# Kernel tuning notes

Hardware: AMD Instinct MI355X
Metric: run time of the kernel (lower is better)

Reference implementation:

```python
import math
import jax, jax.numpy as jnp
import numpy as np

B, S, D, H = 2, 2048, 1024, 16
HD = D // H  # 64


def setup_inputs() -> dict:
    key = jax.random.key(0)
    k = jax.random.split(key, 8)
    x = jax.random.normal(k[0], (B, S, D), dtype=jnp.float32)
    # RoPE tables: inv_freq over half dim, emb = concat(freqs, freqs)
    inv_freq = 1.0 / (10000.0 ** (jnp.arange(0, HD, 2, dtype=jnp.float32) / HD))
    pos = jnp.arange(S, dtype=jnp.float32)
    freqs = pos[:, None] * inv_freq[None, :]            # [S, HD/2]
    emb = jnp.concatenate([freqs, freqs], axis=-1)      # [S, HD]
    cos = jnp.cos(emb)[:, None, :]                      # [S, 1, HD] broadcasts over [B,S,H,HD]
    sin = jnp.sin(emb)[:, None, :]
    # causal additive mask [1, 1, S, S]
    neg = jnp.finfo(jnp.float32).min
    mask = jnp.where(jnp.tril(jnp.ones((S, S), dtype=bool)), 0.0, neg)[None, None]
    scale = 0.02
    wq = jax.random.normal(k[1], (D, D), dtype=jnp.float32) * scale
    wk = jax.random.normal(k[2], (D, D), dtype=jnp.float32) * scale
    wv = jax.random.normal(k[3], (D, D), dtype=jnp.float32) * scale
    wo = jax.random.normal(k[4], (D, D), dtype=jnp.float32) * scale
    return {"x": x, "cos": cos, "sin": sin, "mask": mask,
            "wq": wq, "wk": wk, "wv": wv, "wo": wo}


def rotate_half(t):
    t1, t2 = t[..., : t.shape[-1] // 2], t[..., t.shape[-1] // 2:]
    return jnp.concatenate([-t2, t1], axis=-1)


def reference(x, cos, sin, mask, wq, wk, wv, wo):
    b, s, d = x.shape
    # torch nn.Linear: y = x @ W^T  (W is [out, in])
    q = (x @ wq.T).reshape(b, s, H, HD)
    kk = (x @ wk.T).reshape(b, s, H, HD)
    v = (x @ wv.T).reshape(b, s, H, HD)
    q = q * cos + rotate_half(q) * sin
    kk = kk * cos + rotate_half(kk) * sin
    q = q.transpose(0, 2, 1, 3)   # [b, h, s, hd]
    kk = kk.transpose(0, 2, 1, 3)
    v = v.transpose(0, 2, 1, 3)
    scores = jnp.einsum('bhqd,bhkd->bhqk', q, kk) / math.sqrt(HD)
    scores = scores + mask
    probs = jax.nn.softmax(scores.astype(jnp.float32), axis=-1).astype(q.dtype)
    out = jnp.einsum('bhqk,bhkd->bhqd', probs, v)
    out = out.transpose(0, 2, 1, 3).reshape(b, s, d)
    return out @ wo.T
```

## Files before the change

### kernel.cpp

```cpp
#include <hip/hip_runtime.h>
#include <hip/hip_bf16.h>

typedef __hip_bfloat16 bf16;
typedef unsigned short u16;
typedef __attribute__((ext_vector_type(8))) short short8;
typedef __attribute__((ext_vector_type(4))) float floatx4;

constexpr int B_ = 2, S_ = 2048, D_ = 1024, H_ = 16, HD_ = 64;
constexpr int QT = 64, KT = 64, PAD = 72;
constexpr int NQT = S_ / QT;
constexpr int GK = 1024, BK = 64;

__device__ inline float b2f(u16 u) {
    union { unsigned int i; float f; } v; v.i = ((unsigned int)u) << 16; return v.f;
}
__device__ inline u16 f2b(float f) {
    bf16 h = __float2bfloat16(f); return *(u16*)&h;
}

__device__ inline void gl16(const u16* g, u16* l) {
    __builtin_amdgcn_global_load_lds(
        (const __attribute__((address_space(1))) unsigned int*)g,
        (__attribute__((address_space(3))) unsigned int*)l, 16, 0, 0);
}

#define SBAR() __builtin_amdgcn_sched_barrier(0)

__global__ __launch_bounds__(256) void cvt_kernel(
    const float* __restrict__ x,  const float* __restrict__ wq,
    const float* __restrict__ wk, const float* __restrict__ wv,
    const float* __restrict__ wo,
    u16* __restrict__ Xb, u16* __restrict__ Wb)
{
    const size_t c = (size_t)blockIdx.x * 256 + threadIdx.x;
    const float* src; u16* dst; size_t off;
    if (c < (size_t)(1 << 19)) { src = x; dst = Xb; off = c; }
    else {
        const size_t w = c - (1 << 19);
        const int wi = (int)(w >> 17);
        off = w & ((1 << 17) - 1);
        src = (wi == 0) ? wq : (wi == 1) ? wk : (wi == 2) ? wv : wo;
        dst = Wb + ((size_t)wi << 20);
    }
    const float4 a = *(const float4*)(src + off * 8);
    const float4 b = *(const float4*)(src + off * 8 + 4);
    ushort4 u0; u0.x = f2b(a.x); u0.y = f2b(a.y); u0.z = f2b(a.z); u0.w = f2b(a.w);
    ushort4 u1; u1.x = f2b(b.x); u1.y = f2b(b.y); u1.z = f2b(b.z); u1.w = f2b(b.w);
    *(ushort4*)(dst + off * 8)     = u0;
    *(ushort4*)(dst + off * 8 + 4) = u1;
}

__global__ __launch_bounds__(512, 2) void qkv8(
    const u16* __restrict__ Ag, const u16* __restrict__ Wall,
    const float* __restrict__ cosp, const float* __restrict__ sinp,
    bf16* __restrict__ Qo, bf16* __restrict__ Ko, u16* __restrict__ Vt)
{
    extern __shared__ u16 lds[];

    const int wgid = (blockIdx.x & 7) * 24 + (blockIdx.x >> 3);
    const int mt = wgid / 12;
    const int rem = wgid - mt * 12;
    const int nt = rem & 3, z = rem >> 2;

    const u16* W = Wall + ((size_t)z << 20);
    const int m0 = mt * 256, n0 = nt * 256;

    const int tid  = threadIdx.x;
    const int wave = tid >> 6, lane = tid & 63;
    const int quad = lane >> 4, l16 = lane & 15;
    const int wm = wave >> 2, wn = wave & 3;

    const int lr_st = wave * 16 + (lane >> 2);
    const int csrc  = ((lane & 3) ^ ((lane >> 5) << 1)) * 8;
    const int grA   = ((lr_st >> 6) << 7) + (lr_st & 63);
    const int grB   = ((lr_st >> 5) << 6) + (lr_st & 31);

    const int cidx = ((quad ^ (((l16 >> 3) & 1) << 1))) * 8;

    floatx4 acc[8][4] = {};
    short8 af[4][2], bA[2][2], bB[2][2];

    const u16* A_st = Ag + (size_t)(m0 + grA) * GK + csrc;
    const u16* B_st = W  + (size_t)(n0 + grB) * GK + csrc;

    auto stA = [&](int t2, int mh) {
        if (t2 > 15) return;
        const u16* s = A_st + ((size_t)mh * 64) * GK + t2 * 64;
        u16* d = lds + (((t2 & 1) * 2 + mh) * 8192) + wave * 512;
        gl16(s, d);
        gl16(s + 32, d + 4096);
    };
    auto stB = [&](int t2, int nh) {
        if (t2 > 15) return;
        const u16* s = B_st + ((size_t)nh * 32) * GK + t2 * 64;
        u16* d = lds + 32768 + (((t2 & 1) * 2 + nh) * 8192) + wave * 512;
        gl16(s, d);
        gl16(s + 32, d + 4096);
    };
    auto rdA = [&](int sl, int mh) {
        const int base = (sl * 2 + mh) * 8192 + cidx;
#pragma unroll
        for (int mf = 0; mf < 4; ++mf) {
            const int lr = wm * 64 + mf * 16 + l16;
#pragma unroll
            for (int ks = 0; ks < 2; ++ks)
                af[mf][ks] = *(const short8*)&lds[base + ks * 4096 + lr * 32];
        }
    };
    auto rdB = [&](short8 (&bf)[2][2], int sl, int nh) {
        const int base = 32768 + (sl * 2 + nh) * 8192 + cidx;
#pragma unroll
        for (int fn = 0; fn < 2; ++fn) {
            const int lr = wn * 32 + fn * 16 + l16;
#pragma unroll
            for (int ks = 0; ks < 2; ++ks)
                bf[fn][ks] = *(const short8*)&lds[base + ks * 4096 + lr * 32];
        }
    };
    auto mm = [&](int mh, int nh, short8 (&bf)[2][2]) {
#pragma unroll
        for (int mf = 0; mf < 4; ++mf)
#pragma unroll
            for (int fn = 0; fn < 2; ++fn)
#pragma unroll
                for (int ks = 0; ks < 2; ++ks)
                    acc[mh * 4 + mf][nh * 2 + fn] =
                        __builtin_amdgcn_mfma_f32_16x16x32_bf16(
                            af[mf][ks], bf[fn][ks],
                            acc[mh * 4 + mf][nh * 2 + fn], 0, 0, 0);
    };

    stA(0, 0); stB(0, 0); stA(0, 1); stB(0, 1); stA(1, 0); stB(1, 0);
    asm volatile("s_waitcnt vmcnt(4)" ::: "memory");
    SBAR(); __builtin_amdgcn_s_barrier(); SBAR();

    for (int t = 0; t < 16; ++t) {
        const int sl = t & 1;
        rdA(sl, 0); rdB(bA, sl, 0); stA(t + 1, 1);
        SBAR(); __builtin_amdgcn_s_barrier();
        asm volatile("s_waitcnt lgkmcnt(0)" ::: "memory"); SBAR();
        __builtin_amdgcn_s_setprio(1);
        mm(0, 0, bA);
        __builtin_amdgcn_s_setprio(0);
        SBAR(); __builtin_amdgcn_s_barrier(); SBAR();
        rdB(bB, sl, 1); stB(t + 1, 1);
        SBAR(); __builtin_amdgcn_s_barrier();
        asm volatile("s_waitcnt lgkmcnt(0)" ::: "memory"); SBAR();
        __builtin_amdgcn_s_setprio(1);
        mm(0, 1, bB);
        __builtin_amdgcn_s_setprio(0);
        SBAR(); __builtin_amdgcn_s_barrier(); SBAR();
        rdA(sl, 1); stA(t + 2, 0);
        SBAR(); __builtin_amdgcn_s_barrier();
        asm volatile("s_waitcnt lgkmcnt(0)" ::: "memory"); SBAR();
        __builtin_amdgcn_s_setprio(1);
        mm(1, 0, bA);
        __builtin_amdgcn_s_setprio(0);
        SBAR(); __builtin_amdgcn_s_barrier(); SBAR();
        stB(t + 2, 0);
        SBAR(); __builtin_amdgcn_s_barrier();
        asm volatile("s_waitcnt lgkmcnt(0)" ::: "memory"); SBAR();
        __builtin_amdgcn_s_setprio(1);
        mm(1, 1, bB);
        __builtin_amdgcn_s_setprio(0);
        SBAR();
        if (t < 14)       asm volatile("s_waitcnt vmcnt(4)" ::: "memory");
        else if (t == 14) asm volatile("s_waitcnt vmcnt(0)" ::: "memory");
        SBAR(); __builtin_amdgcn_s_barrier(); SBAR();
    }

    const int s0 = m0 & (S_ - 1);
    const int bq = m0 >> 11;
    const int h  = (n0 >> 6) + wn;

    if (z < 2) {
        float* Cs = (float*)lds;
        float* Sn = (float*)(lds + 16384);
        {
            const int rr = tid >> 1;
            const int cc = (tid & 1) * 16;
            const float4* cp = (const float4*)(cosp + (size_t)(s0 + rr) * HD_ + cc);
            const float4* sp = (const float4*)(sinp + (size_t)(s0 + rr) * HD_ + cc);
            float4* cd = (float4*)&Cs[rr * 32 + cc];
            float4* sd = (float4*)&Sn[rr * 32 + cc];
            cd[0] = cp[0]; cd[1] = cp[1]; cd[2] = cp[2]; cd[3] = cp[3];
            sd[0] = sp[0]; sd[1] = sp[1]; sd[2] = sp[2]; sd[3] = sp[3];
        }
        __syncthreads();

        const float scale = (z == 0) ? 0.125f * 1.44269504f : 1.0f;
        bf16* C = (z == 0) ? Qo : Ko;
#pragma unroll
        for (int mf = 0; mf < 8; ++mf)
#pragma unroll
            for (int r = 0; r < 4; ++r) {
                const int mr = wm * 128 + mf * 16 + quad * 4 + r;
                const size_t base = ((size_t)(bq * H_ + h) * S_ + s0 + mr) << 6;
#pragma unroll
                for (int np = 0; np < 2; ++np) {
                    const int d = np * 16 + l16;
                    const float c1 = Cs[mr * 32 + d];
                    const float s1 = Sn[mr * 32 + d];
                    const float q0 = acc[mf][np][r], q1 = acc[mf][np + 2][r];
                    C[base + d]      = __float2bfloat16((q0 * c1 - q1 * s1) * scale);
                    C[base + d + 32] = __float2bfloat16((q1 * c1 + q0 * s1) * scale);
                }
            }
    } else {
        const int bh = bq * H_ + h;
#pragma unroll
        for (int mf = 0; mf < 8; ++mf)
#pragma unroll
            for (int nf = 0; nf < 4; ++nf) {
                const int hd = nf * 16 + l16;
                const int sb = s0 + wm * 128 + mf * 16 + quad * 4;
                ushort4 pk;
                pk.x = f2b(acc[mf][nf][0]); pk.y = f2b(acc[mf][nf][1]);
                pk.z = f2b(acc[mf][nf][2]); pk.w = f2b(acc[mf][nf][3]);
                *(ushort4*)&Vt[((size_t)(bh * HD_ + hd) << 11) + sb] = pk;
            }
    }
}

template <typename TC, int SCATTER, int ROPE, int BN>
__global__ __launch_bounds__(256) void gemm_async(
    const u16* __restrict__ A, const u16* __restrict__ Wb,
    const float* __restrict__ cosp, const float* __restrict__ sinp,
    TC* __restrict__ C0, TC* __restrict__ C1, TC* __restrict__ C2, int N)
{
    constexpr int NT = BN / 32;

    int x, y, z;
    {
        const int xcd = blockIdx.x & 7, idx = blockIdx.x >> 3;
        y = (xcd & 3) * 8 + (idx & 7);
        if (BN == 128) {
            const int xz = (xcd >> 2) * 12 + (idx >> 3);
            x = xz & 7; z = xz >> 3;
        } else {
            x = (xcd >> 2) * 8 + (idx >> 3);
            z = 0;
        }
    }

    const u16* W = Wb + ((size_t)z << 20);
    TC*        C = (z == 0) ? C0 : (z == 1 ? C1 : C2);

    __shared__ __align__(16) u16 As[128 * BK];
    __shared__ __align__(16) u16 Bs[BN * BK];

    const int tid  = threadIdx.x;
    const int wave = tid >> 6, lane = tid & 63;
    const int quad = lane >> 4, l16 = lane & 15;
    const int wm = wave >> 1, wn = wave & 1;
    const int m0 = y * 128, n0 = x * BN;

    const int srl = lane >> 3;
    const int sc  = (lane & 7) ^ srl;

    floatx4 acc[4][NT] = {};

    for (int k0 = 0; k0 < GK; k0 += BK) {
        __syncthreads();
#pragma unroll
        for (int j = 0; j < 4; ++j) {
            const int rb = wave * 32 + j * 8;
            gl16(A + (size_t)(m0 + rb + srl) * GK + k0 + sc * 8, &As[rb * BK]);
        }
#pragma unroll
        for (int j = 0; j < BN / 32; ++j) {
            const int rb = wave * (BN / 4) + j * 8;
            gl16(W + (size_t)(n0 + rb + srl) * GK + k0 + sc * 8, &Bs[rb * BK]);
        }
        __syncthreads();

#pragma unroll
        for (int ks = 0; ks < 2; ++ks) {
            short8 af[4], bfr[NT];
#pragma unroll
            for (int mt = 0; mt < 4; ++mt) {
                const int R = wm * 64 + mt * 16 + l16;
                af[mt] = *(const short8*)&As[R * BK + (((ks * 4 + quad) ^ (l16 & 7)) * 8)];
            }
#pragma unroll
            for (int nt = 0; nt < NT; ++nt) {
                const int R = wn * (BN / 2) + nt * 16 + l16;
                bfr[nt] = *(const short8*)&Bs[R * BK + (((ks * 4 + quad) ^ (l16 & 7)) * 8)];
            }
#pragma unroll
            for (int mt = 0; mt < 4; ++mt)
#pragma unroll
                for (int nt = 0; nt < NT; ++nt)
                    acc[mt][nt] = __builtin_amdgcn_mfma_f32_16x16x32_bf16(
                        af[mt], bfr[nt], acc[mt][nt], 0, 0, 0);
        }
    }

    if (ROPE && z < 2) {
    } else if (SCATTER) {
    } else {
#pragma unroll
        for (int mt = 0; mt < 4; ++mt)
#pragma unroll
            for (int nt = 0; nt < NT; ++nt)
#pragma unroll
                for (int r = 0; r < 4; ++r) {
                    const int m = m0 + wm * 64 + mt * 16 + quad * 4 + r;
                    const int n = n0 + wn * (BN / 2) + nt * 16 + l16;
                    ((float*)C)[(size_t)m * N + n] = acc[mt][nt][r];
                }
    }
}

__global__ __launch_bounds__(256) void fa_kernel(
    const u16* __restrict__ Qg, const u16* __restrict__ Kg, const u16* __restrict__ Vt,
    bf16* __restrict__ Og)
{
    __shared__ __align__(16) u16 Kt[2][KT * PAD];
    __shared__ __align__(16) u16 Vs[2][HD_ * PAD];
    __shared__ __align__(16) u16 Pt[4 * 16 * PAD];

    const int flat = blockIdx.x;
    const int bx = flat >> 5;
    const int bh = flat & 31;
    const int b  = bh >> 4, h = bh & 15;
    const int tid  = threadIdx.x;
    const int wave = tid >> 6, lane = tid & 63;
    const int quad = lane >> 4, l16 = lane & 15;
    const int srow = tid >> 2, scol = (tid & 3) * 16;

    for (int half = 0; half < 2; ++half) {
        const int qt = half ? (NQT - 1 - bx) : bx;
        const int qb = qt * QT;

        const u16* qrow = Qg + ((size_t)bh * S_ + qb + wave * 16 + l16) * HD_;
        const short8 aq0 = *(const short8*)(qrow + quad * 8);
        const short8 aq1 = *(const short8*)(qrow + 32 + quad * 8);

        floatx4 oacc[4] = {{0,0,0,0},{0,0,0,0},{0,0,0,0},{0,0,0,0}};
        float lsum = 0.f;

        __syncthreads();
        {
            const u16* kp = Kg + ((size_t)bh * S_ + srow) * HD_ + scol;
            *(short8*)&Kt[0][srow * PAD + scol]     = *(const short8*)kp;
            *(short8*)&Kt[0][srow * PAD + scol + 8] = *(const short8*)(kp + 8);
            const u16* vp = Vt + ((size_t)bh * HD_ + srow) * S_ + scol;
            *(short8*)&Vs[0][srow * PAD + scol]     = *(const short8*)vp;
            *(short8*)&Vs[0][srow * PAD + scol + 8] = *(const short8*)(vp + 8);
        }
        __syncthreads();

        for (int it = 0; it <= qt; ++it) {
            const int  cur = it & 1;
            const bool pf  = (it < qt);
            short8 nk0, nk1, nv0, nv1;
            if (pf) {
                const int kb = (it + 1) * KT;
                const u16* kp = Kg + ((size_t)bh * S_ + kb + srow) * HD_ + scol;
                nk0 = *(const short8*)kp; nk1 = *(const short8*)(kp + 8);
                const u16* vp = Vt + ((size_t)bh * HD_ + srow) * S_ + kb + scol;
                nv0 = *(const short8*)vp; nv1 = *(const short8*)(vp + 8);
            }

            floatx4 sacc[4] = {{0,0,0,0},{0,0,0,0},{0,0,0,0},{0,0,0,0}};
#pragma unroll
            for (int kt = 0; kt < 4; ++kt) {
                const short8 bk0 = *(const short8*)&Kt[cur][(kt * 16 + l16) * PAD + quad * 8];
                const short8 bk1 = *(const short8*)&Kt[cur][(kt * 16 + l16) * PAD + 32 + quad * 8];
                sacc[kt] = __builtin_amdgcn_mfma_f32_16x16x32_bf16(bk0, aq0, sacc[kt], 0, 0, 0);
                sacc[kt] = __builtin_amdgcn_mfma_f32_16x16x32_bf16(bk1, aq1, sacc[kt], 0, 0, 0);
            }

            if (it == qt) {
                const int ql = wave * 16 + l16;
#pragma unroll
                for (int kt = 0; kt < 4; ++kt)
#pragma unroll
                    for (int r = 0; r < 4; ++r)
                        if (kt * 16 + quad * 4 + r > ql) sacc[kt][r] = -1.0e38f;
            }

            float rs = 0.f;
#pragma unroll
            for (int kt = 0; kt < 4; ++kt) {
                const float e0 = __builtin_amdgcn_exp2f(sacc[kt][0]);
                const float e1 = __builtin_amdgcn_exp2f(sacc[kt][1]);
                const float e2 = __builtin_amdgcn_exp2f(sacc[kt][2]);
                const float e3 = __builtin_amdgcn_exp2f(sacc[kt][3]);
                rs += (e0 + e1) + (e2 + e3);
                ushort4 pk; pk.x = f2b(e0); pk.y = f2b(e1); pk.z = f2b(e2); pk.w = f2b(e3);
                *(ushort4*)&Pt[(wave * 16 + l16) * PAD + kt * 16 + quad * 4] = pk;
            }
            rs += __shfl_xor(rs, 16);
            rs += __shfl_xor(rs, 32);
            lsum += rs;

            const short8 ap0 = *(const short8*)&Pt[(wave * 16 + l16) * PAD + quad * 8];
            const short8 ap1 = *(const short8*)&Pt[(wave * 16 + l16) * PAD + 32 + quad * 8];

#pragma unroll
            for (int dt = 0; dt < 4; ++dt) {
                const short8 bv0 = *(const short8*)&Vs[cur][(dt * 16 + l16) * PAD + quad * 8];
                const short8 bv1 = *(const short8*)&Vs[cur][(dt * 16 + l16) * PAD + 32 + quad * 8];
                oacc[dt] = __builtin_amdgcn_mfma_f32_16x16x32_bf16(bv0, ap0, oacc[dt], 0, 0, 0);
                oacc[dt] = __builtin_amdgcn_mfma_f32_16x16x32_bf16(bv1, ap1, oacc[dt], 0, 0, 0);
            }

            if (pf) {
                const int nb = cur ^ 1;
                *(short8*)&Kt[nb][srow * PAD + scol]     = nk0;
                *(short8*)&Kt[nb][srow * PAD + scol + 8] = nk1;
                *(short8*)&Vs[nb][srow * PAD + scol]     = nv0;
                *(short8*)&Vs[nb][srow * PAD + scol + 8] = nv1;
            }
            __syncthreads();
        }

        const float inv = 1.0f / lsum;
        bf16* orow = Og + ((size_t)(b * S_ + qb + wave * 16 + l16)) * D_ + h * HD_;
#pragma unroll
        for (int dt = 0; dt < 4; ++dt) {
            ushort4 pk;
            pk.x = f2b(oacc[dt][0] * inv);
            pk.y = f2b(oacc[dt][1] * inv);
            pk.z = f2b(oacc[dt][2] * inv);
            pk.w = f2b(oacc[dt][3] * inv);
            *(ushort4*)((u16*)orow + dt * 16 + quad * 4) = pk;
        }
    }
}

extern "C" void kernel_launch(void* const* d_in, const int* in_sizes, int n_in,
                              void* d_out, int out_size, void* d_ws, size_t ws_size,
                              hipStream_t stream)
{
    const float* x    = (const float*)d_in[0];
    const float* cosp = (const float*)d_in[1];
    const float* sinp = (const float*)d_in[2];
    const float* wq   = (const float*)d_in[4];
    const float* wk   = (const float*)d_in[5];
    const float* wv   = (const float*)d_in[6];
    const float* wo   = (const float*)d_in[7];
    float* out = (float*)d_out;

    u16* w0 = (u16*)d_ws;
    const size_t NE = (size_t)B_ * S_ * D_;
    u16* Qb  = w0;
    u16* Kb  = w0 + NE;
    u16* Vtb = w0 + 2 * NE;
    u16* Xb  = w0 + 3 * NE;
    u16* Wb  = w0 + 4 * NE;
    u16* Ab  = Xb;
    u16* Wob = Wb + 3 * (1 << 20);

    static bool inited = false;
    if (!inited) {
        hipFuncSetAttribute((const void*)qkv8,
                            hipFuncAttributeMaxDynamicSharedMemorySize, 131072);
        inited = true;
    }

    cvt_kernel<<<4096, 256, 0, stream>>>(x, wq, wk, wv, wo, Xb, Wb);

    qkv8<<<192, 512, 131072, stream>>>(
        Xb, Wb, cosp, sinp, (bf16*)Qb, (bf16*)Kb, Vtb);

    fa_kernel<<<dim3((NQT / 2) * 32, 1, 1), 256, 0, stream>>>(Qb, Kb, Vtb, (bf16*)Ab);

    gemm_async<float, 0, 0, 64><<<512, 256, 0, stream>>>(
        Ab, Wob, cosp, sinp, out, out, out, D_);
}
```

Baseline: 189.3 us.

## Restructure flash attention to 128-row Q tiles with register-resident P

The attention kernel now gives each block 128 query rows, 32 per wave, so every K/V tile loaded into shared memory serves twice as many queries. Blocks are launched heaviest-first in place of the earlier pairing of light and heavy tiles. The probability tile is packed directly into MFMA operand registers rather than round-tripping through shared memory, which relies on a permuted V layout in shared memory. Occupancy is hinted at 2 blocks per SIMD. The costs are higher register pressure, waves that sit idle on partially masked tiles, and less even load balancing than the paired schedule.

```diff
diff --git a/kernel.cpp b/kernel.cpp
--- a/kernel.cpp
+++ b/kernel.cpp
@@ -7,8 +7,7 @@
 typedef __attribute__((ext_vector_type(4))) float floatx4;
 
 constexpr int B_ = 2, S_ = 2048, D_ = 1024, H_ = 16, HD_ = 64;
-constexpr int QT = 64, KT = 64, PAD = 72;
-constexpr int NQT = S_ / QT;
+constexpr int KT = 64, PAD = 72;
 constexpr int GK = 1024, BK = 64;
 
 __device__ inline float b2f(u16 u) {
@@ -296,9 +295,7 @@
         }
     }
 
-    if (ROPE && z < 2) {
-    } else if (SCATTER) {
-    } else {
+    {
 #pragma unroll
         for (int mt = 0; mt < 4; ++mt)
 #pragma unroll
@@ -312,120 +309,144 @@
     }
 }
 
-__global__ __launch_bounds__(256) void fa_kernel(
+__global__ __launch_bounds__(256, 2) void fa_kernel(
     const u16* __restrict__ Qg, const u16* __restrict__ Kg, const u16* __restrict__ Vt,
     bf16* __restrict__ Og)
 {
     __shared__ __align__(16) u16 Kt[2][KT * PAD];
-    __shared__ __align__(16) u16 Vs[2][HD_ * PAD];
-    __shared__ __align__(16) u16 Pt[4 * 16 * PAD];
+    __shared__ __align__(16) u16 Vs[2][KT * PAD];
 
     const int flat = blockIdx.x;
-    const int bx = flat >> 5;
     const int bh = flat & 31;
+    const int qt = (S_ / 128 - 1) - (flat >> 5);
     const int b  = bh >> 4, h = bh & 15;
     const int tid  = threadIdx.x;
     const int wave = tid >> 6, lane = tid & 63;
     const int quad = lane >> 4, l16 = lane & 15;
-    const int srow = tid >> 2, scol = (tid & 3) * 16;
-
-    for (int half = 0; half < 2; ++half) {
-        const int qt = half ? (NQT - 1 - bx) : bx;
-        const int qb = qt * QT;
-
-        const u16* qrow = Qg + ((size_t)bh * S_ + qb + wave * 16 + l16) * HD_;
-        const short8 aq0 = *(const short8*)(qrow + quad * 8);
-        const short8 aq1 = *(const short8*)(qrow + 32 + quad * 8);
-
-        floatx4 oacc[4] = {{0,0,0,0},{0,0,0,0},{0,0,0,0},{0,0,0,0}};
-        float lsum = 0.f;
-
-        __syncthreads();
-        {
-            const u16* kp = Kg + ((size_t)bh * S_ + srow) * HD_ + scol;
-            *(short8*)&Kt[0][srow * PAD + scol]     = *(const short8*)kp;
-            *(short8*)&Kt[0][srow * PAD + scol + 8] = *(const short8*)(kp + 8);
-            const u16* vp = Vt + ((size_t)bh * HD_ + srow) * S_ + scol;
-            *(short8*)&Vs[0][srow * PAD + scol]     = *(const short8*)vp;
-            *(short8*)&Vs[0][srow * PAD + scol + 8] = *(const short8*)(vp + 8);
-        }
-        __syncthreads();
-
-        for (int it = 0; it <= qt; ++it) {
-            const int  cur = it & 1;
-            const bool pf  = (it < qt);
-            short8 nk0, nk1, nv0, nv1;
-            if (pf) {
-                const int kb = (it + 1) * KT;
-                const u16* kp = Kg + ((size_t)bh * S_ + kb + srow) * HD_ + scol;
-                nk0 = *(const short8*)kp; nk1 = *(const short8*)(kp + 8);
-                const u16* vp = Vt + ((size_t)bh * HD_ + srow) * S_ + kb + scol;
-                nv0 = *(const short8*)vp; nv1 = *(const short8*)(vp + 8);
-            }
-
-            floatx4 sacc[4] = {{0,0,0,0},{0,0,0,0},{0,0,0,0},{0,0,0,0}};
+    const int srow = tid >> 2;
+    const int sc4  = tid & 3;
+    const int scol = sc4 * 16;
+    const int vwb  = (sc4 >> 1) * 32 + (sc4 & 1) * 4;
+
+    const int Q0 = qt * 128;
+    const int qrow0 = Q0 + wave * 32;
+
+    union S8U { short8 v; ushort4 q[2]; };
+
+    short8 aq[2][2];
+#pragma unroll
+    for (int qh = 0; qh < 2; ++qh) {
+        const u16* qrow = Qg + ((size_t)bh * S_ + qrow0 + qh * 16 + l16) * HD_;
+        aq[qh][0] = *(const short8*)(qrow + quad * 8);
+        aq[qh][1] = *(const short8*)(qrow + 32 + quad * 8);
+    }
+
+    floatx4 oacc[2][4] = {};
+    float lsum[2] = {0.f, 0.f};
+
+    const int T = 2 * qt + 2;
+
+    {
+        const u16* kp = Kg + ((size_t)bh * S_ + srow) * HD_ + scol;
+        *(short8*)&Kt[0][srow * PAD + scol]     = *(const short8*)kp;
+        *(short8*)&Kt[0][srow * PAD + scol + 8] = *(const short8*)(kp + 8);
+        const u16* vp = Vt + ((size_t)bh * HD_ + srow) * S_ + scol;
+        S8U v0, v1; v0.v = *(const short8*)vp; v1.v = *(const short8*)(vp + 8);
+        *(ushort4*)&Vs[0][srow * PAD + vwb]      = v0.q[0];
+        *(ushort4*)&Vs[0][srow * PAD + vwb + 8]  = v0.q[1];
+        *(ushort4*)&Vs[0][srow * PAD + vwb + 16] = v1.q[0];
+        *(ushort4*)&Vs[0][srow * PAD + vwb + 24] = v1.q[1];
+    }
+    __syncthreads();
+
+    for (int it = 0; it < T; ++it) {
+        const int  cur = it & 1;
+        const bool pf  = (it + 1 < T);
+        const int  kb  = it * KT;
+        short8 nk0, nk1; S8U nv0, nv1;
+        if (pf) {
+            const int kb2 = kb + KT;
+            const u16* kp = Kg + ((size_t)bh * S_ + kb2 + srow) * HD_ + scol;
+            nk0 = *(const short8*)kp; nk1 = *(const short8*)(kp + 8);
+            const u16* vp = Vt + ((size_t)bh * HD_ + srow) * S_ + kb2 + scol;
+            nv0.v = *(const short8*)vp; nv1.v = *(const short8*)(vp + 8);
+        }
+
+        if (kb <= qrow0 + 31) {
+            floatx4 s0[4] = {{0,0,0,0},{0,0,0,0},{0,0,0,0},{0,0,0,0}};
+            floatx4 s1[4] = {{0,0,0,0},{0,0,0,0},{0,0,0,0},{0,0,0,0}};
 #pragma unroll
             for (int kt = 0; kt < 4; ++kt) {
                 const short8 bk0 = *(const short8*)&Kt[cur][(kt * 16 + l16) * PAD + quad * 8];
                 const short8 bk1 = *(const short8*)&Kt[cur][(kt * 16 + l16) * PAD + 32 + quad * 8];
-                sacc[kt] = __builtin_amdgcn_mfma_f32_16x16x32_bf16(bk0, aq0, sacc[kt], 0, 0, 0);
-                sacc[kt] = __builtin_amdgcn_mfma_f32_16x16x32_bf16(bk1, aq1, sacc[kt], 0, 0, 0);
-            }
-
-            if (it == qt) {
-                const int ql = wave * 16 + l16;
+                s0[kt] = __builtin_amdgcn_mfma_f32_16x16x32_bf16(bk0, aq[0][0], s0[kt], 0, 0, 0);
+                s0[kt] = __builtin_amdgcn_mfma_f32_16x16x32_bf16(bk1, aq[0][1], s0[kt], 0, 0, 0);
+                s1[kt] = __builtin_amdgcn_mfma_f32_16x16x32_bf16(bk0, aq[1][0], s1[kt], 0, 0, 0);
+                s1[kt] = __builtin_amdgcn_mfma_f32_16x16x32_bf16(bk1, aq[1][1], s1[kt], 0, 0, 0);
+            }
+
+            if (kb + 32 >= qrow0) {
+                const int t0 = l16 - (kb - qrow0) - quad * 4;
 #pragma unroll
                 for (int kt = 0; kt < 4; ++kt)
 #pragma unroll
-                    for (int r = 0; r < 4; ++r)
-                        if (kt * 16 + quad * 4 + r > ql) sacc[kt][r] = -1.0e38f;
-            }
-
-            float rs = 0.f;
-#pragma unroll
-            for (int kt = 0; kt < 4; ++kt) {
-                const float e0 = __builtin_amdgcn_exp2f(sacc[kt][0]);
-                const float e1 = __builtin_amdgcn_exp2f(sacc[kt][1]);
-                const float e2 = __builtin_amdgcn_exp2f(sacc[kt][2]);
-                const float e3 = __builtin_amdgcn_exp2f(sacc[kt][3]);
-                rs += (e0 + e1) + (e2 + e3);
-                ushort4 pk; pk.x = f2b(e0); pk.y = f2b(e1); pk.z = f2b(e2); pk.w = f2b(e3);
-                *(ushort4*)&Pt[(wave * 16 + l16) * PAD + kt * 16 + quad * 4] = pk;
-            }
-            rs += __shfl_xor(rs, 16);
-            rs += __shfl_xor(rs, 32);
-            lsum += rs;
-
-            const short8 ap0 = *(const short8*)&Pt[(wave * 16 + l16) * PAD + quad * 8];
-            const short8 ap1 = *(const short8*)&Pt[(wave * 16 + l16) * PAD + 32 + quad * 8];
+                    for (int r = 0; r < 4; ++r) {
+                        if (kt * 16 + r > t0)      s0[kt][r] = -1.0e38f;
+                        if (kt * 16 + r > t0 + 16) s1[kt][r] = -1.0e38f;
+                    }
+            }
+
+            short8 a0h0, a0h1, a1h0, a1h1;
+            float rs0 = 0.f, rs1 = 0.f;
+#pragma unroll
+            for (int kt = 0; kt < 4; ++kt)
+#pragma unroll
+                for (int r = 0; r < 4; ++r) {
+                    const float e0 = __builtin_amdgcn_exp2f(s0[kt][r]);
+                    const float e1 = __builtin_amdgcn_exp2f(s1[kt][r]);
+                    rs0 += e0; rs1 += e1;
+                    const int idx = (kt & 1) * 4 + r;
+                    if (kt < 2) { a0h0[idx] = (short)f2b(e0); a1h0[idx] = (short)f2b(e1); }
+                    else        { a0h1[idx] = (short)f2b(e0); a1h1[idx] = (short)f2b(e1); }
+                }
+            rs0 += __shfl_xor(rs0, 16); rs0 += __shfl_xor(rs0, 32);
+            rs1 += __shfl_xor(rs1, 16); rs1 += __shfl_xor(rs1, 32);
+            lsum[0] += rs0; lsum[1] += rs1;
 
 #pragma unroll
             for (int dt = 0; dt < 4; ++dt) {
                 const short8 bv0 = *(const short8*)&Vs[cur][(dt * 16 + l16) * PAD + quad * 8];
                 const short8 bv1 = *(const short8*)&Vs[cur][(dt * 16 + l16) * PAD + 32 + quad * 8];
-                oacc[dt] = __builtin_amdgcn_mfma_f32_16x16x32_bf16(bv0, ap0, oacc[dt], 0, 0, 0);
-                oacc[dt] = __builtin_amdgcn_mfma_f32_16x16x32_bf16(bv1, ap1, oacc[dt], 0, 0, 0);
-            }
-
-            if (pf) {
-                const int nb = cur ^ 1;
-                *(short8*)&Kt[nb][srow * PAD + scol]     = nk0;
-                *(short8*)&Kt[nb][srow * PAD + scol + 8] = nk1;
-                *(short8*)&Vs[nb][srow * PAD + scol]     = nv0;
-                *(short8*)&Vs[nb][srow * PAD + scol + 8] = nv1;
-            }
-            __syncthreads();
-        }
-
-        const float inv = 1.0f / lsum;
-        bf16* orow = Og + ((size_t)(b * S_ + qb + wave * 16 + l16)) * D_ + h * HD_;
+                oacc[0][dt] = __builtin_amdgcn_mfma_f32_16x16x32_bf16(bv0, a0h0, oacc[0][dt], 0, 0, 0);
+                oacc[0][dt] = __builtin_amdgcn_mfma_f32_16x16x32_bf16(bv1, a0h1, oacc[0][dt], 0, 0, 0);
+                oacc[1][dt] = __builtin_amdgcn_mfma_f32_16x16x32_bf16(bv0, a1h0, oacc[1][dt], 0, 0, 0);
+                oacc[1][dt] = __builtin_amdgcn_mfma_f32_16x16x32_bf16(bv1, a1h1, oacc[1][dt], 0, 0, 0);
+            }
+        }
+
+        if (pf) {
+            const int nb = cur ^ 1;
+            *(short8*)&Kt[nb][srow * PAD + scol]     = nk0;
+            *(short8*)&Kt[nb][srow * PAD + scol + 8] = nk1;
+            *(ushort4*)&Vs[nb][srow * PAD + vwb]      = nv0.q[0];
+            *(ushort4*)&Vs[nb][srow * PAD + vwb + 8]  = nv0.q[1];
+            *(ushort4*)&Vs[nb][srow * PAD + vwb + 16] = nv1.q[0];
+            *(ushort4*)&Vs[nb][srow * PAD + vwb + 24] = nv1.q[1];
+        }
+        __syncthreads();
+    }
+
+#pragma unroll
+    for (int qh = 0; qh < 2; ++qh) {
+        const float inv = 1.0f / lsum[qh];
+        bf16* orow = Og + ((size_t)(b * S_ + qrow0 + qh * 16 + l16)) * D_ + h * HD_;
 #pragma unroll
         for (int dt = 0; dt < 4; ++dt) {
             ushort4 pk;
-            pk.x = f2b(oacc[dt][0] * inv);
-            pk.y = f2b(oacc[dt][1] * inv);
-            pk.z = f2b(oacc[dt][2] * inv);
-            pk.w = f2b(oacc[dt][3] * inv);
+            pk.x = f2b(oacc[qh][dt][0] * inv);
+            pk.y = f2b(oacc[qh][dt][1] * inv);
+            pk.z = f2b(oacc[qh][dt][2] * inv);
+            pk.w = f2b(oacc[qh][dt][3] * inv);
             *(ushort4*)((u16*)orow + dt * 16 + quad * 4) = pk;
         }
     }
@@ -466,7 +487,7 @@
     qkv8<<<192, 512, 131072, stream>>>(
         Xb, Wb, cosp, sinp, (bf16*)Qb, (bf16*)Kb, Vtb);
 
-    fa_kernel<<<dim3((NQT / 2) * 32, 1, 1), 256, 0, stream>>>(Qb, Kb, Vtb, (bf16*)Ab);
+    fa_kernel<<<512, 256, 0, stream>>>(Qb, Kb, Vtb, (bf16*)Ab);
 
     gemm_async<float, 0, 0, 64><<<512, 256, 0, stream>>>(
         Ab, Wob, cosp, sinp, out, out, out, D_);
```

Result: no change. 191.1 us (+1.0%).
